# Performance work log

Hardware: AMD Instinct MI355X
Metric: run time of the kernel (lower is better)

## Reference

```python
import math
import jax, jax.numpy as jnp
import numpy as np

B, N, D = 32, 1025, 768
K, CD, TD = 64, 128, 256  # num_clusters, cluster_dim, token_dim
REG = 0.1
NUM_ITERS = 5


def setup_inputs() -> dict:
    key = jax.random.key(0)
    ks = jax.random.split(key, 8)
    x = jax.random.normal(ks[0], (B, N, D), dtype=jnp.float32)
    # Linear params (torch nn.Linear: y = x @ W.T + b; we store W already transposed as [in, out])
    Wf = jax.random.normal(ks[1], (D, CD), dtype=jnp.float32) / math.sqrt(D)
    bf = jnp.zeros((CD,), dtype=jnp.float32)
    Ws = jax.random.normal(ks[2], (D, K), dtype=jnp.float32) / math.sqrt(D)
    bs = jnp.zeros((K,), dtype=jnp.float32)
    Wt = jax.random.normal(ks[3], (D, TD), dtype=jnp.float32) / math.sqrt(D)
    bt = jnp.zeros((TD,), dtype=jnp.float32)
    anchors = jax.random.normal(ks[4], (K, CD), dtype=jnp.float32) * 0.1
    dust_bin = jnp.float32(1.0)
    sharpness = jnp.float32(5.0)
    return {"x": x, "Wf": Wf, "bf": bf, "Ws": Ws, "bs": bs, "Wt": Wt, "bt": bt,
            "anchors": anchors, "dust_bin": dust_bin, "sharpness": sharpness}


def _log_otp_solver(log_a, log_b, M, num_iters, reg):
    M = M / reg
    u = jnp.zeros_like(log_a)  # [B, K+1]
    v = jnp.zeros_like(log_b)  # [B, N-1]
    for _ in range(num_iters):
        u = log_a - jax.nn.logsumexp(M + v[:, None, :], axis=2)
        v = log_b - jax.nn.logsumexp(M + u[:, :, None], axis=1)
    return M + u[:, :, None] + v[:, None, :]


def reference(x, Wf, bf, Ws, bs, Wt, bt, anchors, dust_bin, sharpness):
    b, n, d = x.shape
    t_global = x[:, 0]            # [B, D]
    fi = x[:, 1:]                 # [B, N-1, D]
    f = fi @ Wf + bf              # [B, N-1, CD]
    s = jnp.swapaxes(fi @ Ws + bs, 1, 2)  # [B, K, N-1]
    t = t_global @ Wt + bt        # [B, TD]
    s = s * sharpness
    dust = jnp.broadcast_to(dust_bin, (b, 1, n - 1))
    s_aug = jnp.concatenate([s, dust], axis=1)  # [B, K+1, N-1]
    log_a = jnp.full((b, K + 1), -math.log(K + 1), dtype=x.dtype)
    log_b = jnp.full((b, n - 1), -math.log(n - 1), dtype=x.dtype)
    log_P = _log_otp_solver(log_a, log_b, s_aug, NUM_ITERS, REG)
    p = jnp.exp(log_P)[:, :-1, :]  # [B, K, N-1]
    # v_agg = sum_n p[b,k,n] * (2*f[b,n,:] - anchors[k,:])  (algebraic rewrite of the broadcast sum)
    v_agg = 2.0 * jnp.einsum('bkn,bnc->bkc', p, f) - p.sum(axis=2)[:, :, None] * anchors[None]
    v_local = v_agg.reshape(b, -1)            # [B, K*CD]
    f_out = jnp.concatenate([t, v_local], axis=-1)
    norm = jnp.maximum(jnp.linalg.norm(f_out, axis=-1, keepdims=True), 1e-12)
    return f_out / norm
```

## Files before the change

kernel.cpp:

```cpp
#include <hip/hip_runtime.h>
#include <math.h>


#define BATCH 32
#define NTOK  1025
#define DIM   768
#define KDIM  64
#define CDIM  128
#define TDIM  256
#define NM1   1024
#define ROWLEN 8448
#define NITER 5
#define INV_REG 10.0f
#define NS_AGG 8
#define LOG_A (-4.17438727f)
#define LOG_B (-6.93147181f)

typedef __attribute__((ext_vector_type(8))) short short8;
typedef __attribute__((ext_vector_type(4))) float floatx4;

typedef __attribute__((address_space(3))) unsigned int lds_uint;
typedef const __attribute__((address_space(1))) unsigned int glb_uint;

__device__ __forceinline__ void gload_lds16(const void* g, void* l) {
    __builtin_amdgcn_global_load_lds((glb_uint*)g, (lds_uint*)l, 16, 0, 0);
}

__device__ __forceinline__ unsigned short bf16_rne(float f) {
    unsigned u = __builtin_bit_cast(unsigned, f);
    unsigned r = u + 0x7FFFu + ((u >> 16) & 1u);
    return (unsigned short)(r >> 16);
}

__device__ __forceinline__ short8 cvt8(float4 a, float4 b) {
    short8 r;
    r[0] = (short)bf16_rne(a.x); r[1] = (short)bf16_rne(a.y);
    r[2] = (short)bf16_rne(a.z); r[3] = (short)bf16_rne(a.w);
    r[4] = (short)bf16_rne(b.x); r[5] = (short)bf16_rne(b.y);
    r[6] = (short)bf16_rne(b.z); r[7] = (short)bf16_rne(b.w);
    return r;
}

__global__ __launch_bounds__(256) void prep(
    const float* __restrict__ Wf, const float* __restrict__ Ws,
    const float* __restrict__ bf, const float* __restrict__ bs,
    const float* __restrict__ x, const float* __restrict__ Wt,
    short* __restrict__ W_pack, float* __restrict__ bias_all,
    float* __restrict__ tpart)
{
    __shared__ float xr[256];
    const int blk = blockIdx.x, tid = threadIdx.x;
    if (blk < 576) {
        int idx = blk * 256 + tid;
        int g    = idx / 6144;
        int rem  = idx - g * 6144;
        int nf   = rem >> 9;
        int rem2 = rem & 511;
        int lane = rem2 >> 3;
        int j    = rem2 & 7;
        int k = g * 32 + (lane >> 4) * 8 + j;
        int c = nf * 16 + (lane & 15);
        float v = (c < CDIM) ? Wf[(size_t)k * CDIM + c] : Ws[(size_t)k * KDIM + (c - CDIM)];
        W_pack[idx] = (short)bf16_rne(v);
        if (idx < 192) bias_all[idx] = (idx < CDIM) ? bf[idx] : bs[idx - CDIM];
    } else {
        int i = blk - 576;
        int b = i / 3, dy = i - b * 3;
        xr[tid] = x[(size_t)b * NTOK * DIM + (size_t)dy * 256 + tid];
        __syncthreads();
        float acc = 0.f;
        const float* wp = Wt + (size_t)dy * 256 * TDIM + tid;
#pragma unroll 8
        for (int d = 0; d < 256; ++d) acc = fmaf(xr[d], wp[(size_t)d * TDIM], acc);
        tpart[((size_t)dy * BATCH + b) * TDIM + tid] = acc;
    }
}

__global__ __launch_bounds__(256, 2) void gemm_fs(
    const float* __restrict__ x, const short* __restrict__ W_pack,
    const float* __restrict__ bias_all, const float* __restrict__ sharp_p,
    unsigned short* __restrict__ fT, float* __restrict__ Mmat)
{
    __shared__ __align__(16) short Bs[12288];
    __shared__ __align__(16) short As[4096];
    const int tid  = threadIdx.x;
    const int wave = tid >> 6, lane = tid & 63;
    const int quad = lane >> 4, lrow = lane & 15;
    const int R = blockIdx.x * 64 + wave * 16;

    const int arow = blockIdx.x * 64 + (tid >> 2);
    const float* asrc = x + ((size_t)(arow >> 10) * NTOK + 1 + (arow & 1023)) * DIM + (tid & 3) * 16;
    const int r    = (tid >> 2) & 15;
    const int seg  = tid & 3;
    const int kk_w = seg >> 1;
    const int q0   = (seg & 1) * 2;
    short* adst0 = &As[(((tid >> 6) * 2 + kk_w) * 64 + q0 * 16 + r) * 8];
    short* adst1 = &As[(((tid >> 6) * 2 + kk_w) * 64 + (q0 + 1) * 16 + r) * 8];

    floatx4 acc[12];
#pragma unroll
    for (int nf = 0; nf < 12; ++nf) acc[nf] = (floatx4){0.f, 0.f, 0.f, 0.f};

    float4 g0 = *(const float4*)(asrc);
    float4 g1 = *(const float4*)(asrc + 4);
    float4 g2 = *(const float4*)(asrc + 8);
    float4 g3 = *(const float4*)(asrc + 12);

    for (int ko = 0; ko < 12; ++ko) {
        __syncthreads();
        const short* bsrc = W_pack + ko * 12288 + tid * 8;
#pragma unroll
        for (int i = 0; i < 6; ++i)
            gload_lds16(bsrc + i * 2048, &Bs[i * 2048 + tid * 8]);
        *(short8*)adst0 = cvt8(g0, g1);
        *(short8*)adst1 = cvt8(g2, g3);
        if (ko < 11) {
            const float* ap = asrc + (ko + 1) * 64;
            g0 = *(const float4*)(ap);
            g1 = *(const float4*)(ap + 4);
            g2 = *(const float4*)(ap + 8);
            g3 = *(const float4*)(ap + 12);
        }
        __syncthreads();
#pragma unroll
        for (int kk = 0; kk < 2; ++kk) {
            short8 af = *(const short8*)&As[((wave * 2 + kk) * 64 + lane) * 8];
#pragma unroll
            for (int nf = 0; nf < 12; ++nf) {
                short8 bf8 = *(const short8*)&Bs[((kk * 12 + nf) * 64 + lane) * 8];
                acc[nf] = __builtin_amdgcn_mfma_f32_16x16x32_bf16(af, bf8, acc[nf], 0, 0, 0);
            }
        }
    }

    const float sc = sharp_p[0] * INV_REG;
    const int bb = R >> 10;
    const int tok = (R & 1023) + quad * 4;
#pragma unroll
    for (int nf = 0; nf < 12; ++nf) {
        const int c = nf * 16 + lrow;
        const float bias = bias_all[c];
        if (nf < 8) {
            ushort4 w;
            w.x = bf16_rne(acc[nf][0] + bias);
            w.y = bf16_rne(acc[nf][1] + bias);
            w.z = bf16_rne(acc[nf][2] + bias);
            w.w = bf16_rne(acc[nf][3] + bias);
            *(ushort4*)(fT + ((size_t)bb * CDIM + c) * NM1 + tok) = w;
        } else {
            const int k = c - CDIM;
            float4 w = make_float4((acc[nf][0] + bias) * sc, (acc[nf][1] + bias) * sc,
                                   (acc[nf][2] + bias) * sc, (acc[nf][3] + bias) * sc);
            *(float4*)(Mmat + ((size_t)bb * KDIM + k) * NM1 + tok) = w;
        }
    }
}

template<bool FIRST>
__global__ __launch_bounds__(256) void sink_u(
    const float* __restrict__ Mmat, const float* __restrict__ v_in,
    const float* __restrict__ dust_p, float* __restrict__ u_out)
{
    const int wv   = (blockIdx.x << 2) + (threadIdx.x >> 6);
    const int lane = threadIdx.x & 63;
    const int b = wv / 65, k = wv - b * 65;
    const float dustM = dust_p[0] * INV_REG;

    const float4* vp = (const float4*)(v_in + (size_t)b * NM1);
    float xs[16];
    if (k < 64) {
        const float4* Mp = (const float4*)(Mmat + ((size_t)b * KDIM + k) * NM1);
#pragma unroll
        for (int i = 0; i < 4; ++i) {
            float4 mv = Mp[i * 64 + lane];
            float4 vv = FIRST ? make_float4(0.f, 0.f, 0.f, 0.f) : vp[i * 64 + lane];
            xs[i * 4 + 0] = mv.x + vv.x;
            xs[i * 4 + 1] = mv.y + vv.y;
            xs[i * 4 + 2] = mv.z + vv.z;
            xs[i * 4 + 3] = mv.w + vv.w;
        }
    } else {
#pragma unroll
        for (int i = 0; i < 4; ++i) {
            float4 vv = FIRST ? make_float4(0.f, 0.f, 0.f, 0.f) : vp[i * 64 + lane];
            xs[i * 4 + 0] = dustM + vv.x;
            xs[i * 4 + 1] = dustM + vv.y;
            xs[i * 4 + 2] = dustM + vv.z;
            xs[i * 4 + 3] = dustM + vv.w;
        }
    }
    float m = xs[0];
#pragma unroll
    for (int i = 1; i < 16; ++i) m = fmaxf(m, xs[i]);
#pragma unroll
    for (int off = 1; off < 64; off <<= 1) m = fmaxf(m, __shfl_xor(m, off));
    float S = 0.f;
#pragma unroll
    for (int i = 0; i < 16; ++i) S += __expf(xs[i] - m);
#pragma unroll
    for (int off = 1; off < 64; off <<= 1) S += __shfl_xor(S, off);
    if (lane == 0) u_out[wv] = LOG_A - (m + __logf(S));
}

__global__ __launch_bounds__(128) void sink_v(
    const float* __restrict__ Mmat, const float* __restrict__ u_in,
    const float* __restrict__ dust_p, float* __restrict__ v_out)
{
    __shared__ float us[65];
    const int b = blockIdx.x, tid = threadIdx.x;
    const int n = blockIdx.y * 128 + tid;
    if (tid < 65) us[tid] = u_in[b * 65 + tid];
    __syncthreads();
    const float* Mb = Mmat + (size_t)b * KDIM * NM1 + n;
    float xs[64];
#pragma unroll
    for (int k = 0; k < 64; ++k) xs[k] = Mb[(size_t)k * NM1] + us[k];
    const float xd = dust_p[0] * INV_REG + us[64];
    float m = xd;
#pragma unroll
    for (int k = 0; k < 64; ++k) m = fmaxf(m, xs[k]);
    float S = __expf(xd - m);
#pragma unroll
    for (int k = 0; k < 64; ++k) S += __expf(xs[k] - m);
    v_out[(size_t)b * NM1 + n] = LOG_B - (m + __logf(S));
}

__global__ __launch_bounds__(256) void aggregate(
    const float* __restrict__ Mmat, const unsigned short* __restrict__ fT,
    const float* __restrict__ u_in, const float* __restrict__ v_in,
    float* __restrict__ vpart, float* __restrict__ rspart)
{
    __shared__ float us[KDIM];
    __shared__ float vsh[128];
    const int b = blockIdx.x, ns = blockIdx.y;
    const int tid = threadIdx.x;
    const int wave = tid >> 6, lane = tid & 63;
    const int quad = lane >> 4, lrow = lane & 15;

    if (tid < 64) us[tid] = u_in[b * 65 + tid];
    else if (tid < 192) vsh[tid - 64] = v_in[(size_t)b * NM1 + ns * 128 + (tid - 64)];
    __syncthreads();

    const int krow = wave * 16 + lrow;
    const float uk = us[krow];
    const float* Mrow = Mmat + ((size_t)b * KDIM + krow) * NM1 + ns * 128 + quad * 8;
    const unsigned short* fbase = fT + ((size_t)b * CDIM + lrow) * NM1 + ns * 128 + quad * 8;

    floatx4 acc[8];
#pragma unroll
    for (int nf = 0; nf < 8; ++nf) acc[nf] = (floatx4){0.f, 0.f, 0.f, 0.f};
    float rs = 0.f;

#pragma unroll
    for (int step = 0; step < 4; ++step) {
        const float* mp = Mrow + step * 32;
        float4 m0 = *(const float4*)(mp);
        float4 m1 = *(const float4*)(mp + 4);
        const int tb = step * 32 + quad * 8;
        float p[8];
        p[0] = __expf(m0.x + uk + vsh[tb + 0]);
        p[1] = __expf(m0.y + uk + vsh[tb + 1]);
        p[2] = __expf(m0.z + uk + vsh[tb + 2]);
        p[3] = __expf(m0.w + uk + vsh[tb + 3]);
        p[4] = __expf(m1.x + uk + vsh[tb + 4]);
        p[5] = __expf(m1.y + uk + vsh[tb + 5]);
        p[6] = __expf(m1.z + uk + vsh[tb + 6]);
        p[7] = __expf(m1.w + uk + vsh[tb + 7]);
        short8 afrag;
#pragma unroll
        for (int j = 0; j < 8; ++j) {
            rs += p[j];
            afrag[j] = (short)bf16_rne(p[j]);
        }
#pragma unroll
        for (int nf = 0; nf < 8; ++nf) {
            short8 bfrag = *(const short8*)(fbase + (size_t)nf * 16 * NM1 + step * 32);
            acc[nf] = __builtin_amdgcn_mfma_f32_16x16x32_bf16(afrag, bfrag, acc[nf], 0, 0, 0);
        }
    }

    rs += __shfl_xor(rs, 16);
    rs += __shfl_xor(rs, 32);
    if (lane < 16) rspart[(ns * BATCH + b) * KDIM + krow] = rs;

    float* vp = vpart + (size_t)(ns * BATCH + b) * (KDIM * CDIM);
#pragma unroll
    for (int nf = 0; nf < 8; ++nf) {
        const int c = nf * 16 + lrow;
#pragma unroll
        for (int j = 0; j < 4; ++j)
            vp[(size_t)(wave * 16 + quad * 4 + j) * CDIM + c] = acc[nf][j];
    }
}

__global__ __launch_bounds__(1024) void finalize_all(
    const float* __restrict__ vpart, const float* __restrict__ rspart,
    const float* __restrict__ anchors, const float* __restrict__ tpart,
    const float* __restrict__ bt, float* __restrict__ out)
{
    __shared__ float rstot[KDIM];
    __shared__ float red[16];
    __shared__ float sc_sh;
    const int b = blockIdx.x, tid = threadIdx.x;
    const int lane = tid & 63, wave = tid >> 6;

    if (tid < KDIM) {
        float s = 0.f;
#pragma unroll
        for (int ns = 0; ns < NS_AGG; ++ns)
            s += rspart[(ns * BATCH + b) * KDIM + tid];
        rstot[tid] = s;
    }
    __syncthreads();

    const size_t e0 = (size_t)tid * 8;
    float4 s0 = make_float4(0.f, 0.f, 0.f, 0.f);
    float4 s1 = make_float4(0.f, 0.f, 0.f, 0.f);
#pragma unroll
    for (int ns = 0; ns < NS_AGG; ++ns) {
        const float* vp = vpart + (size_t)(ns * BATCH + b) * (KDIM * CDIM) + e0;
        float4 a = *(const float4*)(vp);
        float4 c = *(const float4*)(vp + 4);
        s0.x += a.x; s0.y += a.y; s0.z += a.z; s0.w += a.w;
        s1.x += c.x; s1.y += c.y; s1.z += c.z; s1.w += c.w;
    }
    const float rsv = rstot[tid >> 4];
    float4 a0 = *(const float4*)(anchors + e0);
    float4 a1 = *(const float4*)(anchors + e0 + 4);
    float4 v0, v1;
    v0.x = 2.f * s0.x - rsv * a0.x;  v0.y = 2.f * s0.y - rsv * a0.y;
    v0.z = 2.f * s0.z - rsv * a0.z;  v0.w = 2.f * s0.w - rsv * a0.w;
    v1.x = 2.f * s1.x - rsv * a1.x;  v1.y = 2.f * s1.y - rsv * a1.y;
    v1.z = 2.f * s1.z - rsv * a1.z;  v1.w = 2.f * s1.w - rsv * a1.w;
    float ss = v0.x*v0.x + v0.y*v0.y + v0.z*v0.z + v0.w*v0.w
             + v1.x*v1.x + v1.y*v1.y + v1.z*v1.z + v1.w*v1.w;

    float t = 0.f;
    if (tid < TDIM) {
        t = bt[tid];
#pragma unroll
        for (int s = 0; s < 3; ++s) t += tpart[((size_t)s * BATCH + b) * TDIM + tid];
        ss += t * t;
    }

#pragma unroll
    for (int off = 32; off > 0; off >>= 1) ss += __shfl_down(ss, off);
    if (lane == 0) red[wave] = ss;
    __syncthreads();
    if (tid == 0) {
        float tot = 0.f;
#pragma unroll
        for (int i = 0; i < 16; ++i) tot += red[i];
        sc_sh = 1.f / fmaxf(sqrtf(tot), 1e-12f);
    }
    __syncthreads();
    const float scale = sc_sh;

    float* orow = out + (size_t)b * ROWLEN;
    if (tid < TDIM) orow[tid] = t * scale;
    v0.x *= scale; v0.y *= scale; v0.z *= scale; v0.w *= scale;
    v1.x *= scale; v1.y *= scale; v1.z *= scale; v1.w *= scale;
    *(float4*)&orow[TDIM + e0]     = v0;
    *(float4*)&orow[TDIM + e0 + 4] = v1;
}

extern "C" void kernel_launch(void* const* d_in, const int* in_sizes, int n_in,
                              void* d_out, int out_size, void* d_ws, size_t ws_size,
                              hipStream_t stream)
{
    const float* x       = (const float*)d_in[0];
    const float* Wf      = (const float*)d_in[1];
    const float* bf      = (const float*)d_in[2];
    const float* Ws      = (const float*)d_in[3];
    const float* bs      = (const float*)d_in[4];
    const float* Wt      = (const float*)d_in[5];
    const float* bt      = (const float*)d_in[6];
    const float* anchors = (const float*)d_in[7];
    const float* dust    = (const float*)d_in[8];
    const float* sharp   = (const float*)d_in[9];
    float* out = (float*)d_out;

    char* base = (char*)d_ws;
    short* W_pack        = (short*)base;
    float* bias_all      = (float*)(base + 294912);
    float* Mmat          = bias_all + 192;
    unsigned short* fT   = (unsigned short*)(Mmat + (size_t)BATCH * KDIM * NM1);
    float* u_buf         = (float*)(fT + (size_t)BATCH * CDIM * NM1);
    float* v_buf         = u_buf + BATCH * 65;
    float* vpart         = v_buf + BATCH * NM1;
    float* rspart        = vpart + (size_t)NS_AGG * BATCH * KDIM * CDIM;
    float* tpart         = rspart + NS_AGG * BATCH * KDIM;

    hipLaunchKernelGGL(prep, dim3(672), dim3(256), 0, stream,
                       Wf, Ws, bf, bs, x, Wt, W_pack, bias_all, tpart);
    hipLaunchKernelGGL(gemm_fs, dim3(512), dim3(256), 0, stream,
                       x, W_pack, bias_all, sharp, fT, Mmat);

    hipLaunchKernelGGL(HIP_KERNEL_NAME(sink_u<true>), dim3(520), dim3(256), 0, stream,
                       Mmat, v_buf, dust, u_buf);
    hipLaunchKernelGGL(sink_v, dim3(BATCH, 8), dim3(128), 0, stream,
                       Mmat, u_buf, dust, v_buf);
    for (int it = 1; it < NITER; ++it) {
        hipLaunchKernelGGL(HIP_KERNEL_NAME(sink_u<false>), dim3(520), dim3(256), 0, stream,
                           Mmat, v_buf, dust, u_buf);
        hipLaunchKernelGGL(sink_v, dim3(BATCH, 8), dim3(128), 0, stream,
                           Mmat, u_buf, dust, v_buf);
    }

    hipLaunchKernelGGL(aggregate, dim3(BATCH, NS_AGG), dim3(256), 0, stream,
                       Mmat, fT, u_buf, v_buf, vpart, rspart);
    hipLaunchKernelGGL(finalize_all, dim3(BATCH), dim3(1024), 0, stream,
                       vpart, rspart, anchors, tpart, bt, out);
}
```

Baseline: 243.8 us.

## Fuse Sinkhorn iterations, aggregation and finalize into one cooperative persistent kernel

Replaces the ten sink_u/sink_v launches plus the aggregate and finalize kernels with a single cooperative kernel of 256 blocks. Each block keeps its slice of M in registers across all iterations and computes the v update locally. Only the row logsumexp partials are exchanged through global memory, with one grid-wide sync per iteration. This removes repeated re-reads of M and the per-launch overhead, at the cost of grid syncs and a grid limited to one block per CU.

```diff
diff --git a/kernel.cpp b/kernel.cpp
--- a/kernel.cpp
+++ b/kernel.cpp
@@ -1,5 +1,8 @@
 #include <hip/hip_runtime.h>
+#include <hip/hip_cooperative_groups.h>
 #include <math.h>
+
+namespace cg = cooperative_groups;
 
 
 #define BATCH 32
@@ -156,212 +159,231 @@
     }
 }
 
-template<bool FIRST>
-__global__ __launch_bounds__(256) void sink_u(
-    const float* __restrict__ Mmat, const float* __restrict__ v_in,
-    const float* __restrict__ dust_p, float* __restrict__ u_out)
+__global__ __launch_bounds__(256, 1) void sink_agg(
+    const float* __restrict__ Mmat, const unsigned short* __restrict__ fT,
+    const float* __restrict__ dust_p, const float* __restrict__ anchors,
+    const float* __restrict__ tpart, const float* __restrict__ bt,
+    float* __restrict__ part, float* __restrict__ vpart,
+    float* __restrict__ rspart, float* __restrict__ out)
 {
-    const int wv   = (blockIdx.x << 2) + (threadIdx.x >> 6);
-    const int lane = threadIdx.x & 63;
-    const int b = wv / 65, k = wv - b * 65;
-    const float dustM = dust_p[0] * INV_REG;
-
-    const float4* vp = (const float4*)(v_in + (size_t)b * NM1);
-    float xs[16];
-    if (k < 64) {
-        const float4* Mp = (const float4*)(Mmat + ((size_t)b * KDIM + k) * NM1);
-#pragma unroll
-        for (int i = 0; i < 4; ++i) {
-            float4 mv = Mp[i * 64 + lane];
-            float4 vv = FIRST ? make_float4(0.f, 0.f, 0.f, 0.f) : vp[i * 64 + lane];
-            xs[i * 4 + 0] = mv.x + vv.x;
-            xs[i * 4 + 1] = mv.y + vv.y;
-            xs[i * 4 + 2] = mv.z + vv.z;
-            xs[i * 4 + 3] = mv.w + vv.w;
-        }
-    } else {
-#pragma unroll
-        for (int i = 0; i < 4; ++i) {
-            float4 vv = FIRST ? make_float4(0.f, 0.f, 0.f, 0.f) : vp[i * 64 + lane];
-            xs[i * 4 + 0] = dustM + vv.x;
-            xs[i * 4 + 1] = dustM + vv.y;
-            xs[i * 4 + 2] = dustM + vv.z;
-            xs[i * 4 + 3] = dustM + vv.w;
-        }
-    }
-    float m = xs[0];
-#pragma unroll
-    for (int i = 1; i < 16; ++i) m = fmaxf(m, xs[i]);
-#pragma unroll
-    for (int off = 1; off < 64; off <<= 1) m = fmaxf(m, __shfl_xor(m, off));
-    float S = 0.f;
-#pragma unroll
-    for (int i = 0; i < 16; ++i) S += __expf(xs[i] - m);
-#pragma unroll
-    for (int off = 1; off < 64; off <<= 1) S += __shfl_xor(S, off);
-    if (lane == 0) u_out[wv] = LOG_A - (m + __logf(S));
-}
-
-__global__ __launch_bounds__(128) void sink_v(
-    const float* __restrict__ Mmat, const float* __restrict__ u_in,
-    const float* __restrict__ dust_p, float* __restrict__ v_out)
-{
+    cg::grid_group grid = cg::this_grid();
     __shared__ float us[65];
-    const int b = blockIdx.x, tid = threadIdx.x;
-    const int n = blockIdx.y * 128 + tid;
-    if (tid < 65) us[tid] = u_in[b * 65 + tid];
-    __syncthreads();
-    const float* Mb = Mmat + (size_t)b * KDIM * NM1 + n;
-    float xs[64];
-#pragma unroll
-    for (int k = 0; k < 64; ++k) xs[k] = Mb[(size_t)k * NM1] + us[k];
-    const float xd = dust_p[0] * INV_REG + us[64];
-    float m = xd;
-#pragma unroll
-    for (int k = 0; k < 64; ++k) m = fmaxf(m, xs[k]);
-    float S = __expf(xd - m);
-#pragma unroll
-    for (int k = 0; k < 64; ++k) S += __expf(xs[k] - m);
-    v_out[(size_t)b * NM1 + n] = LOG_B - (m + __logf(S));
-}
-
-__global__ __launch_bounds__(256) void aggregate(
-    const float* __restrict__ Mmat, const unsigned short* __restrict__ fT,
-    const float* __restrict__ u_in, const float* __restrict__ v_in,
-    float* __restrict__ vpart, float* __restrict__ rspart)
-{
-    __shared__ float us[KDIM];
-    __shared__ float vsh[128];
-    const int b = blockIdx.x, ns = blockIdx.y;
+    __shared__ __align__(16) float vsh[128];
+    __shared__ float wv[4][128][2];
+    __shared__ float rstot[64];
+    __shared__ float redf[4];
+    __shared__ float scsh;
+
+    const int blk = blockIdx.x;
+    const int b = blk >> 3, ns = blk & 7;
     const int tid = threadIdx.x;
     const int wave = tid >> 6, lane = tid & 63;
     const int quad = lane >> 4, lrow = lane & 15;
-
-    if (tid < 64) us[tid] = u_in[b * 65 + tid];
-    else if (tid < 192) vsh[tid - 64] = v_in[(size_t)b * NM1 + ns * 128 + (tid - 64)];
+    const int krow = wave * 16 + lrow;
+    const float dustM = dust_p[0] * INV_REG;
+
+    float mreg[32];
+    {
+        const float* Mrow = Mmat + ((size_t)b * KDIM + krow) * NM1 + ns * 128 + quad * 8;
+#pragma unroll
+        for (int s = 0; s < 4; ++s) {
+            float4 a = *(const float4*)(Mrow + s * 32);
+            float4 c = *(const float4*)(Mrow + s * 32 + 4);
+            mreg[s*8+0]=a.x; mreg[s*8+1]=a.y; mreg[s*8+2]=a.z; mreg[s*8+3]=a.w;
+            mreg[s*8+4]=c.x; mreg[s*8+5]=c.y; mreg[s*8+6]=c.z; mreg[s*8+7]=c.w;
+        }
+    }
+    if (tid < 128) vsh[tid] = 0.f;
     __syncthreads();
 
-    const int krow = wave * 16 + lrow;
-    const float uk = us[krow];
-    const float* Mrow = Mmat + ((size_t)b * KDIM + krow) * NM1 + ns * 128 + quad * 8;
-    const unsigned short* fbase = fT + ((size_t)b * CDIM + lrow) * NM1 + ns * 128 + quad * 8;
-
-    floatx4 acc[8];
-#pragma unroll
-    for (int nf = 0; nf < 8; ++nf) acc[nf] = (floatx4){0.f, 0.f, 0.f, 0.f};
-    float rs = 0.f;
-
-#pragma unroll
-    for (int step = 0; step < 4; ++step) {
-        const float* mp = Mrow + step * 32;
-        float4 m0 = *(const float4*)(mp);
-        float4 m1 = *(const float4*)(mp + 4);
-        const int tb = step * 32 + quad * 8;
-        float p[8];
-        p[0] = __expf(m0.x + uk + vsh[tb + 0]);
-        p[1] = __expf(m0.y + uk + vsh[tb + 1]);
-        p[2] = __expf(m0.z + uk + vsh[tb + 2]);
-        p[3] = __expf(m0.w + uk + vsh[tb + 3]);
-        p[4] = __expf(m1.x + uk + vsh[tb + 4]);
-        p[5] = __expf(m1.y + uk + vsh[tb + 5]);
-        p[6] = __expf(m1.z + uk + vsh[tb + 6]);
-        p[7] = __expf(m1.w + uk + vsh[tb + 7]);
-        short8 afrag;
-#pragma unroll
-        for (int j = 0; j < 8; ++j) {
-            rs += p[j];
-            afrag[j] = (short)bf16_rne(p[j]);
-        }
+    for (int it = 0; it < NITER; ++it) {
+        float xs[32];
+#pragma unroll
+        for (int s = 0; s < 4; ++s) {
+            const int tb = s * 32 + quad * 8;
+            float4 v0 = *(const float4*)&vsh[tb];
+            float4 v1 = *(const float4*)&vsh[tb + 4];
+            xs[s*8+0]=mreg[s*8+0]+v0.x; xs[s*8+1]=mreg[s*8+1]+v0.y;
+            xs[s*8+2]=mreg[s*8+2]+v0.z; xs[s*8+3]=mreg[s*8+3]+v0.w;
+            xs[s*8+4]=mreg[s*8+4]+v1.x; xs[s*8+5]=mreg[s*8+5]+v1.y;
+            xs[s*8+6]=mreg[s*8+6]+v1.z; xs[s*8+7]=mreg[s*8+7]+v1.w;
+        }
+        float mx = xs[0];
+#pragma unroll
+        for (int i = 1; i < 32; ++i) mx = fmaxf(mx, xs[i]);
+        mx = fmaxf(mx, __shfl_xor(mx, 16));
+        mx = fmaxf(mx, __shfl_xor(mx, 32));
+        float S = 0.f;
+#pragma unroll
+        for (int i = 0; i < 32; ++i) S += __expf(xs[i] - mx);
+        S += __shfl_xor(S, 16);
+        S += __shfl_xor(S, 32);
+        float2* pb = (float2*)part + ((size_t)((it & 1) * BATCH + b) * NS_AGG + ns) * 65;
+        if (quad == 0) pb[krow] = make_float2(mx, S);
+        if (wave == 0) {
+            float v0 = vsh[lane], v1 = vsh[64 + lane];
+            float md = fmaxf(v0, v1);
+#pragma unroll
+            for (int off = 1; off < 64; off <<= 1) md = fmaxf(md, __shfl_xor(md, off));
+            float Sd = __expf(v0 - md) + __expf(v1 - md);
+#pragma unroll
+            for (int off = 1; off < 64; off <<= 1) Sd += __shfl_xor(Sd, off);
+            if (lane == 0) pb[64] = make_float2(dustM + md, Sd);
+        }
+        __threadfence();
+        grid.sync();
+        if (tid < 65) {
+            const float2* pr = (const float2*)part + ((size_t)((it & 1) * BATCH + b) * NS_AGG) * 65 + tid;
+            float2 pv[8];
+            float M2 = -3.4e38f;
+#pragma unroll
+            for (int q = 0; q < 8; ++q) { pv[q] = pr[q * 65]; M2 = fmaxf(M2, pv[q].x); }
+            float S2 = 0.f;
+#pragma unroll
+            for (int q = 0; q < 8; ++q) S2 += pv[q].y * __expf(pv[q].x - M2);
+            us[tid] = LOG_A - (M2 + __logf(S2));
+        }
+        __syncthreads();
+        const float uk = us[krow];
+#pragma unroll
+        for (int s = 0; s < 4; ++s) {
+#pragma unroll
+            for (int j = 0; j < 8; ++j) {
+                float x = mreg[s*8+j] + uk;
+                float m2 = x;
+                m2 = fmaxf(m2, __shfl_xor(m2, 1));
+                m2 = fmaxf(m2, __shfl_xor(m2, 2));
+                m2 = fmaxf(m2, __shfl_xor(m2, 4));
+                m2 = fmaxf(m2, __shfl_xor(m2, 8));
+                float e = __expf(x - m2);
+                e += __shfl_xor(e, 1);
+                e += __shfl_xor(e, 2);
+                e += __shfl_xor(e, 4);
+                e += __shfl_xor(e, 8);
+                if (lrow == 0) {
+                    wv[wave][s*32 + quad*8 + j][0] = m2;
+                    wv[wave][s*32 + quad*8 + j][1] = e;
+                }
+            }
+        }
+        __syncthreads();
+        if (tid < 128) {
+            const float xd = dustM + us[64];
+            float m3 = xd;
+#pragma unroll
+            for (int w = 0; w < 4; ++w) m3 = fmaxf(m3, wv[w][tid][0]);
+            float S3 = __expf(xd - m3);
+#pragma unroll
+            for (int w = 0; w < 4; ++w) S3 += wv[w][tid][1] * __expf(wv[w][tid][0] - m3);
+            vsh[tid] = LOG_B - (m3 + __logf(S3));
+        }
+        __syncthreads();
+    }
+
+    {
+        const float uk = us[krow];
+        const unsigned short* fbase = fT + ((size_t)b * CDIM + lrow) * NM1 + ns * 128 + quad * 8;
+        floatx4 acc[8];
+#pragma unroll
+        for (int nf = 0; nf < 8; ++nf) acc[nf] = (floatx4){0.f, 0.f, 0.f, 0.f};
+        float rs = 0.f;
+#pragma unroll
+        for (int s = 0; s < 4; ++s) {
+            const int tb = s * 32 + quad * 8;
+            float4 v0 = *(const float4*)&vsh[tb];
+            float4 v1 = *(const float4*)&vsh[tb + 4];
+            float p[8];
+            p[0] = __expf(mreg[s*8+0] + uk + v0.x);
+            p[1] = __expf(mreg[s*8+1] + uk + v0.y);
+            p[2] = __expf(mreg[s*8+2] + uk + v0.z);
+            p[3] = __expf(mreg[s*8+3] + uk + v0.w);
+            p[4] = __expf(mreg[s*8+4] + uk + v1.x);
+            p[5] = __expf(mreg[s*8+5] + uk + v1.y);
+            p[6] = __expf(mreg[s*8+6] + uk + v1.z);
+            p[7] = __expf(mreg[s*8+7] + uk + v1.w);
+            short8 afrag;
+#pragma unroll
+            for (int j = 0; j < 8; ++j) {
+                rs += p[j];
+                afrag[j] = (short)bf16_rne(p[j]);
+            }
+#pragma unroll
+            for (int nf = 0; nf < 8; ++nf) {
+                short8 bfrag = *(const short8*)(fbase + (size_t)nf * 16 * NM1 + s * 32);
+                acc[nf] = __builtin_amdgcn_mfma_f32_16x16x32_bf16(afrag, bfrag, acc[nf], 0, 0, 0);
+            }
+        }
+        rs += __shfl_xor(rs, 16);
+        rs += __shfl_xor(rs, 32);
+        if (lane < 16) rspart[(ns * BATCH + b) * KDIM + krow] = rs;
+
+        float* vp = vpart + (size_t)(ns * BATCH + b) * (KDIM * CDIM);
 #pragma unroll
         for (int nf = 0; nf < 8; ++nf) {
-            short8 bfrag = *(const short8*)(fbase + (size_t)nf * 16 * NM1 + step * 32);
-            acc[nf] = __builtin_amdgcn_mfma_f32_16x16x32_bf16(afrag, bfrag, acc[nf], 0, 0, 0);
-        }
-    }
-
-    rs += __shfl_xor(rs, 16);
-    rs += __shfl_xor(rs, 32);
-    if (lane < 16) rspart[(ns * BATCH + b) * KDIM + krow] = rs;
-
-    float* vp = vpart + (size_t)(ns * BATCH + b) * (KDIM * CDIM);
-#pragma unroll
-    for (int nf = 0; nf < 8; ++nf) {
-        const int c = nf * 16 + lrow;
-#pragma unroll
-        for (int j = 0; j < 4; ++j)
-            vp[(size_t)(wave * 16 + quad * 4 + j) * CDIM + c] = acc[nf][j];
-    }
-}
-
-__global__ __launch_bounds__(1024) void finalize_all(
-    const float* __restrict__ vpart, const float* __restrict__ rspart,
-    const float* __restrict__ anchors, const float* __restrict__ tpart,
-    const float* __restrict__ bt, float* __restrict__ out)
-{
-    __shared__ float rstot[KDIM];
-    __shared__ float red[16];
-    __shared__ float sc_sh;
-    const int b = blockIdx.x, tid = threadIdx.x;
-    const int lane = tid & 63, wave = tid >> 6;
-
-    if (tid < KDIM) {
-        float s = 0.f;
-#pragma unroll
-        for (int ns = 0; ns < NS_AGG; ++ns)
-            s += rspart[(ns * BATCH + b) * KDIM + tid];
-        rstot[tid] = s;
-    }
-    __syncthreads();
-
-    const size_t e0 = (size_t)tid * 8;
-    float4 s0 = make_float4(0.f, 0.f, 0.f, 0.f);
-    float4 s1 = make_float4(0.f, 0.f, 0.f, 0.f);
-#pragma unroll
-    for (int ns = 0; ns < NS_AGG; ++ns) {
-        const float* vp = vpart + (size_t)(ns * BATCH + b) * (KDIM * CDIM) + e0;
-        float4 a = *(const float4*)(vp);
-        float4 c = *(const float4*)(vp + 4);
-        s0.x += a.x; s0.y += a.y; s0.z += a.z; s0.w += a.w;
-        s1.x += c.x; s1.y += c.y; s1.z += c.z; s1.w += c.w;
-    }
-    const float rsv = rstot[tid >> 4];
-    float4 a0 = *(const float4*)(anchors + e0);
-    float4 a1 = *(const float4*)(anchors + e0 + 4);
-    float4 v0, v1;
-    v0.x = 2.f * s0.x - rsv * a0.x;  v0.y = 2.f * s0.y - rsv * a0.y;
-    v0.z = 2.f * s0.z - rsv * a0.z;  v0.w = 2.f * s0.w - rsv * a0.w;
-    v1.x = 2.f * s1.x - rsv * a1.x;  v1.y = 2.f * s1.y - rsv * a1.y;
-    v1.z = 2.f * s1.z - rsv * a1.z;  v1.w = 2.f * s1.w - rsv * a1.w;
-    float ss = v0.x*v0.x + v0.y*v0.y + v0.z*v0.z + v0.w*v0.w
-             + v1.x*v1.x + v1.y*v1.y + v1.z*v1.z + v1.w*v1.w;
-
-    float t = 0.f;
-    if (tid < TDIM) {
-        t = bt[tid];
-#pragma unroll
-        for (int s = 0; s < 3; ++s) t += tpart[((size_t)s * BATCH + b) * TDIM + tid];
+            const int c = nf * 16 + lrow;
+#pragma unroll
+            for (int j = 0; j < 4; ++j)
+                vp[(size_t)(wave * 16 + quad * 4 + j) * CDIM + c] = acc[nf][j];
+        }
+    }
+    __threadfence();
+    grid.sync();
+
+    if (blk < BATCH) {
+        const int b2 = blk;
+        if (tid < KDIM) {
+            float s = 0.f;
+#pragma unroll
+            for (int n2 = 0; n2 < NS_AGG; ++n2)
+                s += rspart[(n2 * BATCH + b2) * KDIM + tid];
+            rstot[tid] = s;
+        }
+        __syncthreads();
+        const int e0 = tid * 32;
+        float4 s4[8];
+#pragma unroll
+        for (int i = 0; i < 8; ++i) s4[i] = make_float4(0.f, 0.f, 0.f, 0.f);
+#pragma unroll
+        for (int n2 = 0; n2 < NS_AGG; ++n2) {
+            const float* vp = vpart + (size_t)(n2 * BATCH + b2) * (KDIM * CDIM) + e0;
+#pragma unroll
+            for (int i = 0; i < 8; ++i) {
+                float4 a = *(const float4*)(vp + i * 4);
+                s4[i].x += a.x; s4[i].y += a.y; s4[i].z += a.z; s4[i].w += a.w;
+            }
+        }
+        const float rsv = rstot[tid >> 2];
+        float ss = 0.f;
+#pragma unroll
+        for (int i = 0; i < 8; ++i) {
+            float4 a = *(const float4*)(anchors + e0 + i * 4);
+            s4[i].x = 2.f * s4[i].x - rsv * a.x;
+            s4[i].y = 2.f * s4[i].y - rsv * a.y;
+            s4[i].z = 2.f * s4[i].z - rsv * a.z;
+            s4[i].w = 2.f * s4[i].w - rsv * a.w;
+            ss += s4[i].x*s4[i].x + s4[i].y*s4[i].y + s4[i].z*s4[i].z + s4[i].w*s4[i].w;
+        }
+        float t = bt[tid];
+#pragma unroll
+        for (int s3 = 0; s3 < 3; ++s3) t += tpart[((size_t)s3 * BATCH + b2) * TDIM + tid];
         ss += t * t;
-    }
-
-#pragma unroll
-    for (int off = 32; off > 0; off >>= 1) ss += __shfl_down(ss, off);
-    if (lane == 0) red[wave] = ss;
-    __syncthreads();
-    if (tid == 0) {
-        float tot = 0.f;
-#pragma unroll
-        for (int i = 0; i < 16; ++i) tot += red[i];
-        sc_sh = 1.f / fmaxf(sqrtf(tot), 1e-12f);
-    }
-    __syncthreads();
-    const float scale = sc_sh;
-
-    float* orow = out + (size_t)b * ROWLEN;
-    if (tid < TDIM) orow[tid] = t * scale;
-    v0.x *= scale; v0.y *= scale; v0.z *= scale; v0.w *= scale;
-    v1.x *= scale; v1.y *= scale; v1.z *= scale; v1.w *= scale;
-    *(float4*)&orow[TDIM + e0]     = v0;
-    *(float4*)&orow[TDIM + e0 + 4] = v1;
+#pragma unroll
+        for (int off = 1; off < 64; off <<= 1) ss += __shfl_xor(ss, off);
+        if (lane == 0) redf[wave] = ss;
+        __syncthreads();
+        if (tid == 0)
+            scsh = 1.f / fmaxf(sqrtf(redf[0] + redf[1] + redf[2] + redf[3]), 1e-12f);
+        __syncthreads();
+        const float scale = scsh;
+        float* orow = out + (size_t)b2 * ROWLEN;
+        orow[tid] = t * scale;
+#pragma unroll
+        for (int i = 0; i < 8; ++i) {
+            float4 r = s4[i];
+            r.x *= scale; r.y *= scale; r.z *= scale; r.w *= scale;
+            *(float4*)&orow[TDIM + e0 + i * 4] = r;
+        }
+    }
 }
 
 extern "C" void kernel_launch(void* const* d_in, const int* in_sizes, int n_in,
@@ -385,9 +407,8 @@
     float* bias_all      = (float*)(base + 294912);
     float* Mmat          = bias_all + 192;
     unsigned short* fT   = (unsigned short*)(Mmat + (size_t)BATCH * KDIM * NM1);
-    float* u_buf         = (float*)(fT + (size_t)BATCH * CDIM * NM1);
-    float* v_buf         = u_buf + BATCH * 65;
-    float* vpart         = v_buf + BATCH * NM1;
+    float* part          = (float*)(fT + (size_t)BATCH * CDIM * NM1);
+    float* vpart         = part + 2 * BATCH * NS_AGG * 65 * 2;
     float* rspart        = vpart + (size_t)NS_AGG * BATCH * KDIM * CDIM;
     float* tpart         = rspart + NS_AGG * BATCH * KDIM;
 
@@ -396,19 +417,11 @@
     hipLaunchKernelGGL(gemm_fs, dim3(512), dim3(256), 0, stream,
                        x, W_pack, bias_all, sharp, fT, Mmat);
 
-    hipLaunchKernelGGL(HIP_KERNEL_NAME(sink_u<true>), dim3(520), dim3(256), 0, stream,
-                       Mmat, v_buf, dust, u_buf);
-    hipLaunchKernelGGL(sink_v, dim3(BATCH, 8), dim3(128), 0, stream,
-                       Mmat, u_buf, dust, v_buf);
-    for (int it = 1; it < NITER; ++it) {
-        hipLaunchKernelGGL(HIP_KERNEL_NAME(sink_u<false>), dim3(520), dim3(256), 0, stream,
-                           Mmat, v_buf, dust, u_buf);
-        hipLaunchKernelGGL(sink_v, dim3(BATCH, 8), dim3(128), 0, stream,
-                           Mmat, u_buf, dust, v_buf);
-    }
-
-    hipLaunchKernelGGL(aggregate, dim3(BATCH, NS_AGG), dim3(256), 0, stream,
-                       Mmat, fT, u_buf, v_buf, vpart, rspart);
-    hipLaunchKernelGGL(finalize_all, dim3(BATCH), dim3(1024), 0, stream,
-                       vpart, rspart, anchors, tpart, bt, out);
-}
+    const float* Mmat_c = Mmat;
+    const unsigned short* fT_c = fT;
+    const float* tpart_c = tpart;
+    void* kargs[] = { (void*)&Mmat_c, (void*)&fT_c, (void*)&dust, (void*)&anchors,
+                      (void*)&tpart_c, (void*)&bt, (void*)&part, (void*)&vpart,
+                      (void*)&rspart, (void*)&out };
+    hipLaunchCooperativeKernel((void*)sink_agg, dim3(256), dim3(256), kargs, 0, stream);
+}
```

New measurement: 616.1 us. +152.7%, slower.

## Fuse Sinkhorn iterations, aggregation and finalize into one per-batch kernel

Applied to the files above, without the earlier changes.

Replaces the ten sink_u/sink_v launches plus the aggregate and finalize kernels with a single kernel that runs one 1024-thread block per batch. Each block keeps its M slice in registers and holds u/v in LDS. It runs all iterations with only block-level syncs, then builds the P tile in LDS for the MFMA aggregation and normalizes in place. This removes launch overhead, repeated global reads of M, and the partial-sum buffers. In exchange only 32 blocks run on the whole GPU, which leaves most CUs idle and adds heavy register pressure.

```diff
diff --git a/kernel.cpp b/kernel.cpp
--- a/kernel.cpp
+++ b/kernel.cpp
@@ -12,7 +12,6 @@
 #define ROWLEN 8448
 #define NITER 5
 #define INV_REG 10.0f
-#define NS_AGG 8
 #define LOG_A (-4.17438727f)
 #define LOG_B (-6.93147181f)
 
@@ -156,212 +155,185 @@
     }
 }
 
-template<bool FIRST>
-__global__ __launch_bounds__(256) void sink_u(
-    const float* __restrict__ Mmat, const float* __restrict__ v_in,
-    const float* __restrict__ dust_p, float* __restrict__ u_out)
+__global__ __launch_bounds__(1024, 1) void solve_b(
+    const float* __restrict__ Mmat, const unsigned short* __restrict__ fT,
+    const float* __restrict__ dust_p, const float* __restrict__ anchors,
+    const float* __restrict__ tpart, const float* __restrict__ bt,
+    float* __restrict__ out)
 {
-    const int wv   = (blockIdx.x << 2) + (threadIdx.x >> 6);
-    const int lane = threadIdx.x & 63;
-    const int b = wv / 65, k = wv - b * 65;
-    const float dustM = dust_p[0] * INV_REG;
-
-    const float4* vp = (const float4*)(v_in + (size_t)b * NM1);
-    float xs[16];
-    if (k < 64) {
-        const float4* Mp = (const float4*)(Mmat + ((size_t)b * KDIM + k) * NM1);
-#pragma unroll
-        for (int i = 0; i < 4; ++i) {
-            float4 mv = Mp[i * 64 + lane];
-            float4 vv = FIRST ? make_float4(0.f, 0.f, 0.f, 0.f) : vp[i * 64 + lane];
-            xs[i * 4 + 0] = mv.x + vv.x;
-            xs[i * 4 + 1] = mv.y + vv.y;
-            xs[i * 4 + 2] = mv.z + vv.z;
-            xs[i * 4 + 3] = mv.w + vv.w;
-        }
-    } else {
-#pragma unroll
-        for (int i = 0; i < 4; ++i) {
-            float4 vv = FIRST ? make_float4(0.f, 0.f, 0.f, 0.f) : vp[i * 64 + lane];
-            xs[i * 4 + 0] = dustM + vv.x;
-            xs[i * 4 + 1] = dustM + vv.y;
-            xs[i * 4 + 2] = dustM + vv.z;
-            xs[i * 4 + 3] = dustM + vv.w;
-        }
-    }
-    float m = xs[0];
-#pragma unroll
-    for (int i = 1; i < 16; ++i) m = fmaxf(m, xs[i]);
-#pragma unroll
-    for (int off = 1; off < 64; off <<= 1) m = fmaxf(m, __shfl_xor(m, off));
-    float S = 0.f;
-#pragma unroll
-    for (int i = 0; i < 16; ++i) S += __expf(xs[i] - m);
-#pragma unroll
-    for (int off = 1; off < 64; off <<= 1) S += __shfl_xor(S, off);
-    if (lane == 0) u_out[wv] = LOG_A - (m + __logf(S));
-}
-
-__global__ __launch_bounds__(128) void sink_v(
-    const float* __restrict__ Mmat, const float* __restrict__ u_in,
-    const float* __restrict__ dust_p, float* __restrict__ v_out)
-{
+    __shared__ __align__(16) char scratch[131072];
+    __shared__ float vsh[NM1];
     __shared__ float us[65];
-    const int b = blockIdx.x, tid = threadIdx.x;
-    const int n = blockIdx.y * 128 + tid;
-    if (tid < 65) us[tid] = u_in[b * 65 + tid];
-    __syncthreads();
-    const float* Mb = Mmat + (size_t)b * KDIM * NM1 + n;
-    float xs[64];
-#pragma unroll
-    for (int k = 0; k < 64; ++k) xs[k] = Mb[(size_t)k * NM1] + us[k];
-    const float xd = dust_p[0] * INV_REG + us[64];
-    float m = xd;
-#pragma unroll
-    for (int k = 0; k < 64; ++k) m = fmaxf(m, xs[k]);
-    float S = __expf(xd - m);
-#pragma unroll
-    for (int k = 0; k < 64; ++k) S += __expf(xs[k] - m);
-    v_out[(size_t)b * NM1 + n] = LOG_B - (m + __logf(S));
-}
-
-__global__ __launch_bounds__(256) void aggregate(
-    const float* __restrict__ Mmat, const unsigned short* __restrict__ fT,
-    const float* __restrict__ u_in, const float* __restrict__ v_in,
-    float* __restrict__ vpart, float* __restrict__ rspart)
-{
-    __shared__ float us[KDIM];
-    __shared__ float vsh[128];
-    const int b = blockIdx.x, ns = blockIdx.y;
-    const int tid = threadIdx.x;
-    const int wave = tid >> 6, lane = tid & 63;
-    const int quad = lane >> 4, lrow = lane & 15;
-
-    if (tid < 64) us[tid] = u_in[b * 65 + tid];
-    else if (tid < 192) vsh[tid - 64] = v_in[(size_t)b * NM1 + ns * 128 + (tid - 64)];
-    __syncthreads();
-
-    const int krow = wave * 16 + lrow;
-    const float uk = us[krow];
-    const float* Mrow = Mmat + ((size_t)b * KDIM + krow) * NM1 + ns * 128 + quad * 8;
-    const unsigned short* fbase = fT + ((size_t)b * CDIM + lrow) * NM1 + ns * 128 + quad * 8;
-
-    floatx4 acc[8];
-#pragma unroll
-    for (int nf = 0; nf < 8; ++nf) acc[nf] = (floatx4){0.f, 0.f, 0.f, 0.f};
-    float rs = 0.f;
-
-#pragma unroll
-    for (int step = 0; step < 4; ++step) {
-        const float* mp = Mrow + step * 32;
-        float4 m0 = *(const float4*)(mp);
-        float4 m1 = *(const float4*)(mp + 4);
-        const int tb = step * 32 + quad * 8;
-        float p[8];
-        p[0] = __expf(m0.x + uk + vsh[tb + 0]);
-        p[1] = __expf(m0.y + uk + vsh[tb + 1]);
-        p[2] = __expf(m0.z + uk + vsh[tb + 2]);
-        p[3] = __expf(m0.w + uk + vsh[tb + 3]);
-        p[4] = __expf(m1.x + uk + vsh[tb + 4]);
-        p[5] = __expf(m1.y + uk + vsh[tb + 5]);
-        p[6] = __expf(m1.z + uk + vsh[tb + 6]);
-        p[7] = __expf(m1.w + uk + vsh[tb + 7]);
-        short8 afrag;
-#pragma unroll
-        for (int j = 0; j < 8; ++j) {
-            rs += p[j];
-            afrag[j] = (short)bf16_rne(p[j]);
-        }
-#pragma unroll
-        for (int nf = 0; nf < 8; ++nf) {
-            short8 bfrag = *(const short8*)(fbase + (size_t)nf * 16 * NM1 + step * 32);
-            acc[nf] = __builtin_amdgcn_mfma_f32_16x16x32_bf16(afrag, bfrag, acc[nf], 0, 0, 0);
-        }
-    }
-
-    rs += __shfl_xor(rs, 16);
-    rs += __shfl_xor(rs, 32);
-    if (lane < 16) rspart[(ns * BATCH + b) * KDIM + krow] = rs;
-
-    float* vp = vpart + (size_t)(ns * BATCH + b) * (KDIM * CDIM);
-#pragma unroll
-    for (int nf = 0; nf < 8; ++nf) {
-        const int c = nf * 16 + lrow;
-#pragma unroll
-        for (int j = 0; j < 4; ++j)
-            vp[(size_t)(wave * 16 + quad * 4 + j) * CDIM + c] = acc[nf][j];
-    }
-}
-
-__global__ __launch_bounds__(1024) void finalize_all(
-    const float* __restrict__ vpart, const float* __restrict__ rspart,
-    const float* __restrict__ anchors, const float* __restrict__ tpart,
-    const float* __restrict__ bt, float* __restrict__ out)
-{
     __shared__ float rstot[KDIM];
     __shared__ float red[16];
-    __shared__ float sc_sh;
-    const int b = blockIdx.x, tid = threadIdx.x;
-    const int lane = tid & 63, wave = tid >> 6;
-
-    if (tid < KDIM) {
-        float s = 0.f;
-#pragma unroll
-        for (int ns = 0; ns < NS_AGG; ++ns)
-            s += rspart[(ns * BATCH + b) * KDIM + tid];
-        rstot[tid] = s;
-    }
+    __shared__ float scsh;
+
+    const int b = blockIdx.x;
+    const int tid = threadIdx.x;
+    const int w = tid >> 6, lane = tid & 63;
+    const float dustM = dust_p[0] * INV_REG;
+
+    float mreg[64];
+    {
+        const float* Mb = Mmat + ((size_t)b * KDIM + 4 * w) * NM1 + lane;
+#pragma unroll
+        for (int r = 0; r < 4; ++r)
+#pragma unroll
+            for (int j = 0; j < 16; ++j)
+                mreg[r * 16 + j] = Mb[(size_t)r * NM1 + j * 64];
+    }
+    vsh[tid] = 0.f;
     __syncthreads();
 
-    const size_t e0 = (size_t)tid * 8;
-    float4 s0 = make_float4(0.f, 0.f, 0.f, 0.f);
-    float4 s1 = make_float4(0.f, 0.f, 0.f, 0.f);
-#pragma unroll
-    for (int ns = 0; ns < NS_AGG; ++ns) {
-        const float* vp = vpart + (size_t)(ns * BATCH + b) * (KDIM * CDIM) + e0;
-        float4 a = *(const float4*)(vp);
-        float4 c = *(const float4*)(vp + 4);
-        s0.x += a.x; s0.y += a.y; s0.z += a.z; s0.w += a.w;
-        s1.x += c.x; s1.y += c.y; s1.z += c.z; s1.w += c.w;
-    }
-    const float rsv = rstot[tid >> 4];
-    float4 a0 = *(const float4*)(anchors + e0);
-    float4 a1 = *(const float4*)(anchors + e0 + 4);
-    float4 v0, v1;
-    v0.x = 2.f * s0.x - rsv * a0.x;  v0.y = 2.f * s0.y - rsv * a0.y;
-    v0.z = 2.f * s0.z - rsv * a0.z;  v0.w = 2.f * s0.w - rsv * a0.w;
-    v1.x = 2.f * s1.x - rsv * a1.x;  v1.y = 2.f * s1.y - rsv * a1.y;
-    v1.z = 2.f * s1.z - rsv * a1.z;  v1.w = 2.f * s1.w - rsv * a1.w;
-    float ss = v0.x*v0.x + v0.y*v0.y + v0.z*v0.z + v0.w*v0.w
-             + v1.x*v1.x + v1.y*v1.y + v1.z*v1.z + v1.w*v1.w;
-
+    float2* me = (float2*)scratch;
+    float ur[4];
+
+    for (int it = 0; it < NITER; ++it) {
+        float vv[16];
+#pragma unroll
+        for (int j = 0; j < 16; ++j) vv[j] = vsh[lane + 64 * j];
+#pragma unroll
+        for (int r = 0; r < 4; ++r) {
+            float m = mreg[r * 16 + 0] + vv[0];
+#pragma unroll
+            for (int j = 1; j < 16; ++j) m = fmaxf(m, mreg[r * 16 + j] + vv[j]);
+#pragma unroll
+            for (int off = 1; off < 64; off <<= 1) m = fmaxf(m, __shfl_xor(m, off));
+            float S = 0.f;
+#pragma unroll
+            for (int j = 0; j < 16; ++j) S += __expf(mreg[r * 16 + j] + vv[j] - m);
+#pragma unroll
+            for (int off = 1; off < 64; off <<= 1) S += __shfl_xor(S, off);
+            ur[r] = LOG_A - (m + __logf(S));
+        }
+        if (lane == 0) {
+            us[4 * w + 0] = ur[0]; us[4 * w + 1] = ur[1];
+            us[4 * w + 2] = ur[2]; us[4 * w + 3] = ur[3];
+        }
+        if (w == 0) {
+            float md = vv[0];
+#pragma unroll
+            for (int j = 1; j < 16; ++j) md = fmaxf(md, vv[j]);
+#pragma unroll
+            for (int off = 1; off < 64; off <<= 1) md = fmaxf(md, __shfl_xor(md, off));
+            float Sd = 0.f;
+#pragma unroll
+            for (int j = 0; j < 16; ++j) Sd += __expf(vv[j] - md);
+#pragma unroll
+            for (int off = 1; off < 64; off <<= 1) Sd += __shfl_xor(Sd, off);
+            if (lane == 0) us[64] = LOG_A - (dustM + md + __logf(Sd));
+        }
+#pragma unroll
+        for (int j = 0; j < 16; ++j) {
+            float x0 = mreg[0 * 16 + j] + ur[0];
+            float x1 = mreg[1 * 16 + j] + ur[1];
+            float x2 = mreg[2 * 16 + j] + ur[2];
+            float x3 = mreg[3 * 16 + j] + ur[3];
+            float m4 = fmaxf(fmaxf(x0, x1), fmaxf(x2, x3));
+            float e4 = __expf(x0 - m4) + __expf(x1 - m4)
+                     + __expf(x2 - m4) + __expf(x3 - m4);
+            me[w * 1024 + lane + 64 * j] = make_float2(m4, e4);
+        }
+        __syncthreads();
+        {
+            const float xd = dustM + us[64];
+            float m3 = xd;
+#pragma unroll
+            for (int q = 0; q < 16; ++q) m3 = fmaxf(m3, me[q * 1024 + tid].x);
+            float S3 = __expf(xd - m3);
+#pragma unroll
+            for (int q = 0; q < 16; ++q) {
+                float2 pe = me[q * 1024 + tid];
+                S3 += pe.y * __expf(pe.x - m3);
+            }
+            vsh[tid] = LOG_B - (m3 + __logf(S3));
+        }
+        __syncthreads();
+    }
+
+    unsigned short* ptile = (unsigned short*)scratch;
+    {
+        const int ks = w >> 2;
+#pragma unroll
+        for (int r = 0; r < 4; ++r) {
+            const int k = 4 * w + r;
+            const int lrow = k & 15;
+            float rs = 0.f;
+#pragma unroll
+            for (int j = 0; j < 16; ++j) {
+                const int tok = lane + 64 * j;
+                float p = __expf(mreg[r * 16 + j] + ur[r] + vsh[tok]);
+                rs += p;
+                const int st = tok >> 5, quad = (tok >> 3) & 3, jj = tok & 7;
+                ptile[(((ks * 32 + st) * 64) + quad * 16 + lrow) * 8 + jj] = bf16_rne(p);
+            }
+#pragma unroll
+            for (int off = 1; off < 64; off <<= 1) rs += __shfl_xor(rs, off);
+            if (lane == 0) rstot[k] = rs;
+        }
+    }
+    __syncthreads();
+
+    const int ks2 = w & 3;
+    const int cf0 = (w >> 2) * 2;
+    const int quad = lane >> 4, lrow = lane & 15;
+    floatx4 acc0 = (floatx4){0.f, 0.f, 0.f, 0.f};
+    floatx4 acc1 = (floatx4){0.f, 0.f, 0.f, 0.f};
+    const unsigned short* fb0 = fT + ((size_t)b * CDIM + cf0 * 16 + lrow) * NM1 + quad * 8;
+#pragma unroll
+    for (int st = 0; st < 32; ++st) {
+        short8 af = *(const short8*)&ptile[(((ks2 * 32 + st) * 64) + lane) * 8];
+        short8 b0 = *(const short8*)(fb0 + st * 32);
+        short8 b1 = *(const short8*)(fb0 + (size_t)16 * NM1 + st * 32);
+        acc0 = __builtin_amdgcn_mfma_f32_16x16x32_bf16(af, b0, acc0, 0, 0, 0);
+        acc1 = __builtin_amdgcn_mfma_f32_16x16x32_bf16(af, b1, acc1, 0, 0, 0);
+    }
+
+    float vout[8];
+    float ss = 0.f;
+#pragma unroll
+    for (int t2 = 0; t2 < 2; ++t2) {
+        const int c = (cf0 + t2) * 16 + lrow;
+#pragma unroll
+        for (int j = 0; j < 4; ++j) {
+            const int k = 16 * ks2 + quad * 4 + j;
+            float a = t2 ? acc1[j] : acc0[j];
+            float v = 2.f * a - rstot[k] * anchors[k * CDIM + c];
+            vout[t2 * 4 + j] = v;
+            ss += v * v;
+        }
+    }
     float t = 0.f;
     if (tid < TDIM) {
         t = bt[tid];
 #pragma unroll
-        for (int s = 0; s < 3; ++s) t += tpart[((size_t)s * BATCH + b) * TDIM + tid];
+        for (int s3 = 0; s3 < 3; ++s3) t += tpart[((size_t)s3 * BATCH + b) * TDIM + tid];
         ss += t * t;
     }
-
-#pragma unroll
-    for (int off = 32; off > 0; off >>= 1) ss += __shfl_down(ss, off);
-    if (lane == 0) red[wave] = ss;
+#pragma unroll
+    for (int off = 1; off < 64; off <<= 1) ss += __shfl_xor(ss, off);
+    if (lane == 0) red[w] = ss;
     __syncthreads();
     if (tid == 0) {
         float tot = 0.f;
 #pragma unroll
         for (int i = 0; i < 16; ++i) tot += red[i];
-        sc_sh = 1.f / fmaxf(sqrtf(tot), 1e-12f);
+        scsh = 1.f / fmaxf(sqrtf(tot), 1e-12f);
     }
     __syncthreads();
-    const float scale = sc_sh;
+    const float scale = scsh;
 
     float* orow = out + (size_t)b * ROWLEN;
     if (tid < TDIM) orow[tid] = t * scale;
-    v0.x *= scale; v0.y *= scale; v0.z *= scale; v0.w *= scale;
-    v1.x *= scale; v1.y *= scale; v1.z *= scale; v1.w *= scale;
-    *(float4*)&orow[TDIM + e0]     = v0;
-    *(float4*)&orow[TDIM + e0 + 4] = v1;
+#pragma unroll
+    for (int t2 = 0; t2 < 2; ++t2) {
+        const int c = (cf0 + t2) * 16 + lrow;
+#pragma unroll
+        for (int j = 0; j < 4; ++j) {
+            const int k = 16 * ks2 + quad * 4 + j;
+            orow[TDIM + k * CDIM + c] = vout[t2 * 4 + j] * scale;
+        }
+    }
 }
 
 extern "C" void kernel_launch(void* const* d_in, const int* in_sizes, int n_in,
@@ -385,30 +357,12 @@
     float* bias_all      = (float*)(base + 294912);
     float* Mmat          = bias_all + 192;
     unsigned short* fT   = (unsigned short*)(Mmat + (size_t)BATCH * KDIM * NM1);
-    float* u_buf         = (float*)(fT + (size_t)BATCH * CDIM * NM1);
-    float* v_buf         = u_buf + BATCH * 65;
-    float* vpart         = v_buf + BATCH * NM1;
-    float* rspart        = vpart + (size_t)NS_AGG * BATCH * KDIM * CDIM;
-    float* tpart         = rspart + NS_AGG * BATCH * KDIM;
+    float* tpart         = (float*)(fT + (size_t)BATCH * CDIM * NM1);
 
     hipLaunchKernelGGL(prep, dim3(672), dim3(256), 0, stream,
                        Wf, Ws, bf, bs, x, Wt, W_pack, bias_all, tpart);
     hipLaunchKernelGGL(gemm_fs, dim3(512), dim3(256), 0, stream,
                        x, W_pack, bias_all, sharp, fT, Mmat);
-
-    hipLaunchKernelGGL(HIP_KERNEL_NAME(sink_u<true>), dim3(520), dim3(256), 0, stream,
-                       Mmat, v_buf, dust, u_buf);
-    hipLaunchKernelGGL(sink_v, dim3(BATCH, 8), dim3(128), 0, stream,
-                       Mmat, u_buf, dust, v_buf);
-    for (int it = 1; it < NITER; ++it) {
-        hipLaunchKernelGGL(HIP_KERNEL_NAME(sink_u<false>), dim3(520), dim3(256), 0, stream,
-                           Mmat, v_buf, dust, u_buf);
-        hipLaunchKernelGGL(sink_v, dim3(BATCH, 8), dim3(128), 0, stream,
-                           Mmat, u_buf, dust, v_buf);
-    }
-
-    hipLaunchKernelGGL(aggregate, dim3(BATCH, NS_AGG), dim3(256), 0, stream,
-                       Mmat, fT, u_buf, v_buf, vpart, rspart);
-    hipLaunchKernelGGL(finalize_all, dim3(BATCH), dim3(1024), 0, stream,
-                       vpart, rspart, anchors, tpart, bt, out);
-}
+    hipLaunchKernelGGL(solve_b, dim3(BATCH), dim3(1024), 0, stream,
+                       Mmat, fT, dust, anchors, tpart, bt, out);
+}
```

Result: slower. 287.1 us (+17.8%).
